# Performance work log

Hardware: AMD Instinct MI355X
Metric: run time of the kernel (lower is better)

## Reference

```python
import jax, jax.numpy as jnp
import numpy as np


def setup_inputs() -> dict:
    key = jax.random.key(0)
    ks = jax.random.split(key, 7)
    B, T, N, D, K = 64, 1024, 512, 64, 80
    return {
        "review_seq": jax.random.normal(ks[0], (B, T, D), dtype=jnp.float32),
        "post_seq": jax.random.normal(ks[1], (B, N, D), dtype=jnp.float32),
        "Wl": jax.random.normal(ks[2], (D, D), dtype=jnp.float32) * 0.05,
        "Wr": jax.random.normal(ks[3], (K, D), dtype=jnp.float32) * 0.05,
        "Wp": jax.random.normal(ks[4], (K, D), dtype=jnp.float32) * 0.05,
        "whr": jax.random.normal(ks[5], (1, K), dtype=jnp.float32) * 0.05,
        "whp": jax.random.normal(ks[6], (1, K), dtype=jnp.float32) * 0.05,
    }


def reference(review_seq, post_seq, Wl, Wr, Wp, whr, whp):
    # Affinity matrix: L[b,t,n] = tanh(review[b,t,:] @ Wl @ post[b,n,:])
    L = jnp.tanh(jnp.einsum('btd,dD,bnD->btn', review_seq, Wl, post_seq))
    # Co-attention hidden maps (k x seq)
    Hp = jnp.tanh(jnp.einsum('kd,bnd->bkn', Wp, post_seq)
                  + jnp.einsum('kd,btd,btn->bkn', Wr, review_seq, L))
    Hr = jnp.tanh(jnp.einsum('kd,btd->bkt', Wr, review_seq)
                  + jnp.einsum('kd,bnd,btn->bkt', Wp, post_seq, L))
    # Attention weights over post (n) and review (t) positions
    Ap = jax.nn.softmax(jnp.einsum('k,bkn->bn', whp[0], Hp), axis=-1)
    Ar = jax.nn.softmax(jnp.einsum('k,bkt->bt', whr[0], Hr), axis=-1)
    # Attention-weighted pooling
    co_p = jnp.einsum('bnd,bn->bd', post_seq, Ap)
    co_r = jnp.einsum('btd,bt->bd', review_seq, Ar)
    return jnp.concatenate([co_p, co_r], axis=1)  # [B, 2*D]
```

## Files before the change

kernel.cpp:

```cpp
#include <hip/hip_runtime.h>
#include <hip/hip_bf16.h>
#include <cstdint>

#define DEV __device__ __forceinline__

constexpr int B = 64, T = 1024, N = 512, D = 64, K = 80;

typedef __attribute__((ext_vector_type(8))) short bf16x8;
typedef __attribute__((ext_vector_type(4))) float f32x4;

DEV float fast_tanh(float x) {
    x = fminf(fmaxf(x, -15.f), 15.f);
    float e = __expf(2.f * x);
    return 1.f - 2.f * __builtin_amdgcn_rcpf(e + 1.f);
}

DEV unsigned short f2bf(float f) {
    unsigned int u = __float_as_uint(f);
    unsigned int r = (u + 0x7fffu + ((u >> 16) & 1u)) >> 16;
    return (unsigned short)r;
}
DEV float bf2f(unsigned short s) {
    return __uint_as_float(((unsigned int)s) << 16);
}

DEV unsigned short cvt_bf16(float v) {
    __hip_bfloat16 h = __float2bfloat16(v);
    return *reinterpret_cast<unsigned short*>(&h);
}

DEV void gload16(const unsigned short* src, unsigned short* dst) {
    __builtin_amdgcn_global_load_lds(
        (const __attribute__((address_space(1))) void*)src,
        (__attribute__((address_space(3))) void*)dst,
        16, 0, 0);
}

DEV size_t tix(size_t row, int col, int S8) {
    return (((row >> 4) * S8 + (size_t)(col >> 3)) << 7) + ((row & 15) << 3) + (col & 7);
}

#define MFMA(a, b, c) __builtin_amdgcn_mfma_f32_16x16x32_bf16((a), (b), (c), 0, 0, 0)


DEV void matWl_body(int bid, char* lds, const float* __restrict__ review,
                    const float* __restrict__ Wl,
                    unsigned short* __restrict__ Mhi, unsigned short* __restrict__ Mlo) {
    float (*Wls)[64] = reinterpret_cast<float(*)[64]>(lds);
    float (*Rs)[64]  = reinterpret_cast<float(*)[64]>(lds + 16384);
    int tid = threadIdx.x;
    size_t base = (size_t)bid * 4096;
#pragma unroll
    for (int i = 0; i < 16; i++) {
        int e = tid + i * 256;
        Wls[e >> 6][e & 63] = Wl[e];
        Rs[e >> 6][e & 63] = review[base + e];
    }
    __syncthreads();
    int c = tid & 63, r0 = tid >> 6;
    float acc[16];
#pragma unroll
    for (int i = 0; i < 16; i++) acc[i] = 0.f;
    for (int d = 0; d < 64; d += 2) {
        float w0 = Wls[d][c], w1 = Wls[d + 1][c];
#pragma unroll
        for (int i = 0; i < 16; i++)
            acc[i] += Rs[r0 * 16 + i][d] * w0 + Rs[r0 * 16 + i][d + 1] * w1;
    }
#pragma unroll
    for (int i = 0; i < 16; i++) {
        size_t row = (size_t)bid * 64 + r0 * 16 + i;
        size_t o = tix(row, c, 8);
        unsigned short h = f2bf(acc[i]);
        Mhi[o] = h;
        Mlo[o] = f2bf(acc[i] - bf2f(h));
    }
}

DEV void split_body(int bid, const float* __restrict__ X,
                    unsigned short* __restrict__ Xhi, unsigned short* __restrict__ Xlo) {
    int i = bid * 256 + threadIdx.x;
    float4 v = *reinterpret_cast<const float4*>(X + (size_t)i * 4);
    ushort4 h, lo;
    h.x = f2bf(v.x); lo.x = f2bf(v.x - bf2f(h.x));
    h.y = f2bf(v.y); lo.y = f2bf(v.y - bf2f(h.y));
    h.z = f2bf(v.z); lo.z = f2bf(v.z - bf2f(h.z));
    h.w = f2bf(v.w); lo.w = f2bf(v.w - bf2f(h.w));
    size_t o = tix((size_t)(i >> 4), (i & 15) * 4, 8);
    *reinterpret_cast<ushort4*>(Xhi + o) = h;
    *reinterpret_cast<ushort4*>(Xlo + o) = lo;
}

DEV void proj_body(int sx, int b, char* lds, const float* __restrict__ W,
                   const float* __restrict__ X,
                   unsigned short* __restrict__ Phi, unsigned short* __restrict__ Plo, int S) {
    float (*Ws)[64] = reinterpret_cast<float(*)[64]>(lds);
    float (*Xs)[65] = reinterpret_cast<float(*)[65]>(lds + 20480);
    int tid = threadIdx.x, tx = tid & 63, ty = tid >> 6;
    int s0 = sx * 64;
#pragma unroll
    for (int i = 0; i < 20; i++) { int e = tid + i * 256; Ws[e >> 6][e & 63] = W[e]; }
    const float* Xp = X + ((size_t)b * S + s0) * 64;
#pragma unroll
    for (int i = 0; i < 16; i++) { int e = tid + i * 256; Xs[e >> 6][e & 63] = Xp[e]; }
    __syncthreads();
    float acc[20];
#pragma unroll
    for (int kk = 0; kk < 20; kk++) acc[kk] = 0.f;
    for (int d = 0; d < 64; d += 4) {
        float x0 = Xs[tx][d], x1 = Xs[tx][d + 1], x2 = Xs[tx][d + 2], x3 = Xs[tx][d + 3];
#pragma unroll
        for (int kk = 0; kk < 20; kk++) {
            const float4 w = *reinterpret_cast<const float4*>(&Ws[ty * 20 + kk][d]);
            acc[kk] += w.x * x0 + w.y * x1 + w.z * x2 + w.w * x3;
        }
    }
    int S8 = S >> 3;
#pragma unroll
    for (int kk = 0; kk < 20; kk++) {
        size_t idx = tix((size_t)b * K + ty * 20 + kk, s0 + tx, S8);
        float v = acc[kk];
        unsigned short h = f2bf(v);
        Phi[idx] = h;
        Plo[idx] = f2bf(v - bf2f(h));
    }
}

__global__ __launch_bounds__(256) void k_prelude(
    const float* __restrict__ review, const float* __restrict__ post,
    const float* __restrict__ Wl, const float* __restrict__ Wr,
    const float* __restrict__ Wp,
    unsigned short* __restrict__ Mhi, unsigned short* __restrict__ Mlo,
    unsigned short* __restrict__ PsH, unsigned short* __restrict__ PsL,
    unsigned short* __restrict__ Rhi, unsigned short* __restrict__ Rlo,
    unsigned short* __restrict__ Phi, unsigned short* __restrict__ Plo,
    float* __restrict__ out) {
    __shared__ __align__(16) char lds[37120];
    int bid = blockIdx.x;
    if (bid < 1024) {
        matWl_body(bid, lds, review, Wl, Mhi, Mlo);
    } else if (bid < 3072) {
        split_body(bid - 1024, post, PsH, PsL);
    } else if (bid < 4096) {
        int i = bid - 3072;
        proj_body(i & 15, i >> 4, lds, Wr, review, Rhi, Rlo, T);
    } else if (bid < 4608) {
        int i = bid - 4096;
        proj_body(i & 7, i >> 3, lds, Wp, post, Phi, Plo, N);
    } else {
        int i = bid - 4608;
        out[(size_t)i * 256 + threadIdx.x] = 0.f;
    }
}


DEV void hp_body(int b, int nc0, unsigned short* smem,
                 const unsigned short* __restrict__ Mhi, const unsigned short* __restrict__ Mlo,
                 const unsigned short* __restrict__ PsH, const unsigned short* __restrict__ PsL,
                 const unsigned short* __restrict__ Rhi, const unsigned short* __restrict__ Rlo,
                 const unsigned short* __restrict__ Phi, const unsigned short* __restrict__ Plo,
                 const float* __restrict__ whp, float* __restrict__ logits_p) {
    unsigned short* MH_l = smem;
    unsigned short* ML_l = smem + 4096;
    unsigned short* RH_l = smem + 8192;
    unsigned short* RL_l = smem + 13312;
    typedef unsigned short LtRow[72];
    LtRow* Lt = reinterpret_cast<LtRow*>(smem + 18432);
    int tid = threadIdx.x, l = tid & 63, wv = tid >> 6;
    int lr = l & 15, lg = l >> 4;

    size_t prow = (size_t)b * N + nc0 + wv * 16 + lr;
    size_t p0 = tix(prow, lg * 8, 8), p1 = tix(prow, 32 + lg * 8, 8);
    bf16x8 pah0 = *reinterpret_cast<const bf16x8*>(PsH + p0);
    bf16x8 pah1 = *reinterpret_cast<const bf16x8*>(PsH + p1);
    bf16x8 pal0 = *reinterpret_cast<const bf16x8*>(PsL + p0);
    bf16x8 pal1 = *reinterpret_cast<const bf16x8*>(PsL + p1);

    const unsigned short* srcp[9];
    unsigned short* dstp[9];
    int strd[9];
#pragma unroll
    for (int i = 0; i < 9; i++) {
        int c = wv + i * 4;
        if (c < 8) {
            srcp[i] = Mhi + (size_t)b * T * 64 + c * 512;
            dstp[i] = MH_l + c * 512;
            strd[i] = 4096;
        } else if (c < 16) {
            srcp[i] = Mlo + (size_t)b * T * 64 + (c - 8) * 512;
            dstp[i] = ML_l + (c - 8) * 512;
            strd[i] = 4096;
        } else {
            int j = c - 16, jj = (j < 10) ? j : j - 10;
            int rg = jj >> 1, half = jj & 1;
            srcp[i] = ((j < 10) ? Rhi : Rlo) + (size_t)(b * 5 + rg) * 16384 + half * 512;
            dstp[i] = ((j < 10) ? RH_l : RL_l) + rg * 1024 + half * 512;
            strd[i] = 1024;
        }
        srcp[i] += l * 8;
    }

    f32x4 hp[5];
#pragma unroll
    for (int f = 0; f < 5; f++) hp[f] = (f32x4){0.f, 0.f, 0.f, 0.f};

#pragma unroll
    for (int i = 0; i < 4; i++) { gload16(srcp[i], dstp[i]); srcp[i] += strd[i]; }
    __syncthreads();
#pragma unroll
    for (int i = 4; i < 9; i++) { gload16(srcp[i], dstp[i]); srcp[i] += strd[i]; }

    for (int tt = 0; tt < 16; tt++) {
#pragma unroll
        for (int tf = 0; tf < 4; tf++) {
            int o0 = tf * 1024 + lg * 128 + lr * 8;
            int o1 = tf * 1024 + (4 + lg) * 128 + lr * 8;
            bf16x8 mh0 = *reinterpret_cast<const bf16x8*>(MH_l + o0);
            bf16x8 mh1 = *reinterpret_cast<const bf16x8*>(MH_l + o1);
            bf16x8 ml0 = *reinterpret_cast<const bf16x8*>(ML_l + o0);
            bf16x8 ml1 = *reinterpret_cast<const bf16x8*>(ML_l + o1);
            f32x4 a = (f32x4){0.f, 0.f, 0.f, 0.f};
            a = MFMA(pah0, mh0, a);
            a = MFMA(pah0, ml0, a);
            a = MFMA(pal0, mh0, a);
            a = MFMA(pah1, mh1, a);
            a = MFMA(pah1, ml1, a);
            a = MFMA(pal1, mh1, a);
#pragma unroll
            for (int r = 0; r < 4; r++)
                Lt[wv * 16 + lg * 4 + r][tf * 16 + lr] = cvt_bf16(fast_tanh(a[r]));
        }
        __syncthreads();
        if (tt < 15) {
#pragma unroll
            for (int i = 0; i < 4; i++) { gload16(srcp[i], dstp[i]); srcp[i] += strd[i]; }
        }
        bf16x8 bt0 = *reinterpret_cast<const bf16x8*>(&Lt[wv * 16 + lr][lg * 8]);
        bf16x8 bt1 = *reinterpret_cast<const bf16x8*>(&Lt[wv * 16 + lr][32 + lg * 8]);
#pragma unroll
        for (int kf = 0; kf < 5; kf++) {
            int o0 = kf * 1024 + lg * 128 + lr * 8;
            int o1 = kf * 1024 + (4 + lg) * 128 + lr * 8;
            bf16x8 rh0 = *reinterpret_cast<const bf16x8*>(RH_l + o0);
            bf16x8 rh1 = *reinterpret_cast<const bf16x8*>(RH_l + o1);
            bf16x8 rl0 = *reinterpret_cast<const bf16x8*>(RL_l + o0);
            bf16x8 rl1 = *reinterpret_cast<const bf16x8*>(RL_l + o1);
            hp[kf] = MFMA(rh0, bt0, hp[kf]);
            hp[kf] = MFMA(rl0, bt0, hp[kf]);
            hp[kf] = MFMA(rh1, bt1, hp[kf]);
            hp[kf] = MFMA(rl1, bt1, hp[kf]);
        }
        __syncthreads();
        if (tt < 15) {
#pragma unroll
            for (int i = 4; i < 9; i++) { gload16(srcp[i], dstp[i]); srcp[i] += strd[i]; }
        }
    }

    int n = nc0 + wv * 16 + lr;
    float partial = 0.f;
#pragma unroll
    for (int kf = 0; kf < 5; kf++)
#pragma unroll
        for (int r = 0; r < 4; r++) {
            int k = kf * 16 + lg * 4 + r;
            size_t idx = tix((size_t)b * K + k, n, 64);
            float pp = bf2f(Phi[idx]) + bf2f(Plo[idx]);
            partial += whp[k] * fast_tanh(pp + hp[kf][r]);
        }
    partial += __shfl_xor(partial, 16);
    partial += __shfl_xor(partial, 32);
    if (lg == 0) logits_p[(size_t)b * N + n] = partial;
}

DEV void hr_body(int b, int tc0, unsigned short* smem,
                 const unsigned short* __restrict__ Mhi, const unsigned short* __restrict__ Mlo,
                 const unsigned short* __restrict__ PsH, const unsigned short* __restrict__ PsL,
                 const unsigned short* __restrict__ Phi, const unsigned short* __restrict__ Plo,
                 const unsigned short* __restrict__ Rhi, const unsigned short* __restrict__ Rlo,
                 const float* __restrict__ whr, float* __restrict__ logits_r) {
    unsigned short* PsH_l = smem;
    unsigned short* PsL_l = smem + 4096;
    unsigned short* PpH_l = smem + 8192;
    unsigned short* PpL_l = smem + 13312;
    typedef unsigned short LtRow[72];
    LtRow* Lt = reinterpret_cast<LtRow*>(smem + 18432);
    int tid = threadIdx.x, l = tid & 63, wv = tid >> 6;
    int lr = l & 15, lg = l >> 4;

    size_t mrow = (size_t)b * T + tc0 + wv * 16 + lr;
    size_t m0 = tix(mrow, lg * 8, 8), m1 = tix(mrow, 32 + lg * 8, 8);
    bf16x8 mh0 = *reinterpret_cast<const bf16x8*>(Mhi + m0);
    bf16x8 mh1 = *reinterpret_cast<const bf16x8*>(Mhi + m1);
    bf16x8 ml0 = *reinterpret_cast<const bf16x8*>(Mlo + m0);
    bf16x8 ml1 = *reinterpret_cast<const bf16x8*>(Mlo + m1);

    const unsigned short* srcp[9];
    unsigned short* dstp[9];
    int strd[9];
#pragma unroll
    for (int i = 0; i < 9; i++) {
        int c = wv + i * 4;
        if (c < 8) {
            srcp[i] = PsH + (size_t)b * N * 64 + c * 512;
            dstp[i] = PsH_l + c * 512;
            strd[i] = 4096;
        } else if (c < 16) {
            srcp[i] = PsL + (size_t)b * N * 64 + (c - 8) * 512;
            dstp[i] = PsL_l + (c - 8) * 512;
            strd[i] = 4096;
        } else {
            int j = c - 16, jj = (j < 10) ? j : j - 10;
            int rg = jj >> 1, half = jj & 1;
            srcp[i] = ((j < 10) ? Phi : Plo) + (size_t)(b * 5 + rg) * 8192 + half * 512;
            dstp[i] = ((j < 10) ? PpH_l : PpL_l) + rg * 1024 + half * 512;
            strd[i] = 1024;
        }
        srcp[i] += l * 8;
    }

    f32x4 hr[5];
#pragma unroll
    for (int f = 0; f < 5; f++) hr[f] = (f32x4){0.f, 0.f, 0.f, 0.f};

#pragma unroll
    for (int i = 0; i < 4; i++) { gload16(srcp[i], dstp[i]); srcp[i] += strd[i]; }
    __syncthreads();
#pragma unroll
    for (int i = 4; i < 9; i++) { gload16(srcp[i], dstp[i]); srcp[i] += strd[i]; }

    for (int nt = 0; nt < 8; nt++) {
#pragma unroll
        for (int nf = 0; nf < 4; nf++) {
            int o0 = nf * 1024 + lg * 128 + lr * 8;
            int o1 = nf * 1024 + (4 + lg) * 128 + lr * 8;
            bf16x8 ph0 = *reinterpret_cast<const bf16x8*>(PsH_l + o0);
            bf16x8 ph1 = *reinterpret_cast<const bf16x8*>(PsH_l + o1);
            bf16x8 pl0 = *reinterpret_cast<const bf16x8*>(PsL_l + o0);
            bf16x8 pl1 = *reinterpret_cast<const bf16x8*>(PsL_l + o1);
            f32x4 a = (f32x4){0.f, 0.f, 0.f, 0.f};
            a = MFMA(mh0, ph0, a);
            a = MFMA(mh0, pl0, a);
            a = MFMA(ml0, ph0, a);
            a = MFMA(mh1, ph1, a);
            a = MFMA(mh1, pl1, a);
            a = MFMA(ml1, ph1, a);
#pragma unroll
            for (int r = 0; r < 4; r++)
                Lt[wv * 16 + lg * 4 + r][nf * 16 + lr] = cvt_bf16(fast_tanh(a[r]));
        }
        __syncthreads();
        if (nt < 7) {
#pragma unroll
            for (int i = 0; i < 4; i++) { gload16(srcp[i], dstp[i]); srcp[i] += strd[i]; }
        }
        bf16x8 bt0 = *reinterpret_cast<const bf16x8*>(&Lt[wv * 16 + lr][lg * 8]);
        bf16x8 bt1 = *reinterpret_cast<const bf16x8*>(&Lt[wv * 16 + lr][32 + lg * 8]);
#pragma unroll
        for (int kf = 0; kf < 5; kf++) {
            int o0 = kf * 1024 + lg * 128 + lr * 8;
            int o1 = kf * 1024 + (4 + lg) * 128 + lr * 8;
            bf16x8 qh0 = *reinterpret_cast<const bf16x8*>(PpH_l + o0);
            bf16x8 qh1 = *reinterpret_cast<const bf16x8*>(PpH_l + o1);
            bf16x8 ql0 = *reinterpret_cast<const bf16x8*>(PpL_l + o0);
            bf16x8 ql1 = *reinterpret_cast<const bf16x8*>(PpL_l + o1);
            hr[kf] = MFMA(qh0, bt0, hr[kf]);
            hr[kf] = MFMA(ql0, bt0, hr[kf]);
            hr[kf] = MFMA(qh1, bt1, hr[kf]);
            hr[kf] = MFMA(ql1, bt1, hr[kf]);
        }
        __syncthreads();
        if (nt < 7) {
#pragma unroll
            for (int i = 4; i < 9; i++) { gload16(srcp[i], dstp[i]); srcp[i] += strd[i]; }
        }
    }

    int t = tc0 + wv * 16 + lr;
    float partial = 0.f;
#pragma unroll
    for (int kf = 0; kf < 5; kf++)
#pragma unroll
        for (int r = 0; r < 4; r++) {
            int k = kf * 16 + lg * 4 + r;
            size_t idx = tix((size_t)b * K + k, t, 128);
            float rr = bf2f(Rhi[idx]) + bf2f(Rlo[idx]);
            partial += whr[k] * fast_tanh(rr + hr[kf][r]);
        }
    partial += __shfl_xor(partial, 16);
    partial += __shfl_xor(partial, 32);
    if (lg == 0) logits_r[(size_t)b * T + t] = partial;
}

__global__ __launch_bounds__(256) void k_fused(
    const unsigned short* __restrict__ Mhi, const unsigned short* __restrict__ Mlo,
    const unsigned short* __restrict__ PsH, const unsigned short* __restrict__ PsL,
    const unsigned short* __restrict__ Rhi, const unsigned short* __restrict__ Rlo,
    const unsigned short* __restrict__ Phi, const unsigned short* __restrict__ Plo,
    const float* __restrict__ whp, const float* __restrict__ whr,
    float* __restrict__ logits_p, float* __restrict__ logits_r) {
    __shared__ __align__(16) unsigned short smem[23040];
    int lin = blockIdx.x;
    int x = lin & 7, j = lin >> 3;
    int bg = j / 24, role = j - bg * 24;
    int b = bg * 8 + x;
    if (role < 8) {
        hp_body(b, role * 64, smem, Mhi, Mlo, PsH, PsL, Rhi, Rlo, Phi, Plo, whp, logits_p);
    } else {
        hr_body(b, (role - 8) * 64, smem, Mhi, Mlo, PsH, PsL, Phi, Plo, Rhi, Rlo, whr, logits_r);
    }
}

DEV void softpool_body(const float* __restrict__ logits, const float* __restrict__ X,
                       float* __restrict__ out, int S, int off, int cy,
                       float* sm, float* red) {
    int b = blockIdx.x, tid = threadIdx.x;
    int c0 = cy * 128;
    for (int i = tid; i < S; i += 256) sm[i] = logits[(size_t)b * S + i];
    __syncthreads();
    float m = -1e30f;
    for (int i = tid; i < S; i += 256) m = fmaxf(m, sm[i]);
    red[tid] = m;
    __syncthreads();
    for (int s = 128; s > 0; s >>= 1) {
        if (tid < s) red[tid] = fmaxf(red[tid], red[tid + s]);
        __syncthreads();
    }
    float mx = red[0];
    __syncthreads();
    float psum = 0.f;
    for (int i = tid; i < S; i += 256) {
        float e = __expf(sm[i] - mx);
        sm[i] = e;
        psum += e;
    }
    red[tid] = psum;
    __syncthreads();
    for (int s = 128; s > 0; s >>= 1) {
        if (tid < s) red[tid] += red[tid + s];
        __syncthreads();
    }
    float inv = 1.f / red[0];
    __syncthreads();
    int d = tid & 63, g = tid >> 6;
    float acc = 0.f;
    for (int n = c0 + g; n < c0 + 128; n += 4) acc += sm[n] * X[((size_t)b * S + n) * 64 + d];
    red[tid] = acc * inv;
    __syncthreads();
    if (g == 0)
        atomicAdd(&out[(size_t)b * 128 + off + d],
                  red[d] + red[64 + d] + red[128 + d] + red[192 + d]);
}

__global__ __launch_bounds__(256) void k_softpool2(
    const float* __restrict__ logits_p, const float* __restrict__ logits_r,
    const float* __restrict__ post, const float* __restrict__ review,
    float* __restrict__ out) {
    __shared__ float sm[1024];
    __shared__ float red[256];
    int y = blockIdx.y;
    if (y < N / 128) softpool_body(logits_p, post, out, N, 0, y, sm, red);
    else             softpool_body(logits_r, review, out, T, 64, y - N / 128, sm, red);
}

extern "C" void kernel_launch(void* const* d_in, const int* in_sizes, int n_in,
                              void* d_out, int out_size, void* d_ws, size_t ws_size,
                              hipStream_t stream) {
    const float* review = (const float*)d_in[0];
    const float* post   = (const float*)d_in[1];
    const float* Wl     = (const float*)d_in[2];
    const float* Wr     = (const float*)d_in[3];
    const float* Wp     = (const float*)d_in[4];
    const float* whr    = (const float*)d_in[5];
    const float* whp    = (const float*)d_in[6];
    float* out = (float*)d_out;

    char* p = (char*)d_ws;
    unsigned short* Mhi = (unsigned short*)p;  p += (size_t)B * T * D * 2;
    unsigned short* Mlo = (unsigned short*)p;  p += (size_t)B * T * D * 2;
    unsigned short* PsH = (unsigned short*)p;  p += (size_t)B * N * D * 2;
    unsigned short* PsL = (unsigned short*)p;  p += (size_t)B * N * D * 2;
    unsigned short* Rhi = (unsigned short*)p;  p += (size_t)B * K * T * 2;
    unsigned short* Rlo = (unsigned short*)p;  p += (size_t)B * K * T * 2;
    unsigned short* Phi = (unsigned short*)p;  p += (size_t)B * K * N * 2;
    unsigned short* Plo = (unsigned short*)p;  p += (size_t)B * K * N * 2;
    float* logits_p = (float*)p;        p += (size_t)B * N * 4;
    float* logits_r = (float*)p;        p += (size_t)B * T * 4;

    k_prelude<<<dim3(4640), dim3(256), 0, stream>>>(review, post, Wl, Wr, Wp,
                                                    Mhi, Mlo, PsH, PsL, Rhi, Rlo,
                                                    Phi, Plo, out);
    k_fused<<<dim3(1536), dim3(256), 0, stream>>>(Mhi, Mlo, PsH, PsL, Rhi, Rlo,
                                                  Phi, Plo, whp, whr, logits_p, logits_r);
    k_softpool2<<<dim3(B, 12), dim3(256), 0, stream>>>(logits_p, logits_r, post, review, out);
}
```

Baseline: 139.3 us.

## Fuse softmax pooling into main kernel via last-block counter; add MFMA priority hints

Removes the separate softmax-pool launch. Each batch's 24 blocks in the fused kernel increment a per-batch counter, and the last block to finish computes both softmax poolings for that batch and writes the output directly, with no atomics on the output. The prelude now zeroes the counters instead of the output. s_setprio hints are also placed around the MFMA sections to raise wave priority during compute. The cost is that the pooling work is serialized in a single block per batch, which may create a tail at the end of the kernel.

Result: slower. 353.1 us (+153.5%).

```diff
diff --git a/kernel.cpp b/kernel.cpp
--- a/kernel.cpp
+++ b/kernel.cpp
@@ -134,7 +134,7 @@
     unsigned short* __restrict__ PsH, unsigned short* __restrict__ PsL,
     unsigned short* __restrict__ Rhi, unsigned short* __restrict__ Rlo,
     unsigned short* __restrict__ Phi, unsigned short* __restrict__ Plo,
-    float* __restrict__ out) {
+    int* __restrict__ cnt) {
     __shared__ __align__(16) char lds[37120];
     int bid = blockIdx.x;
     if (bid < 1024) {
@@ -148,8 +148,7 @@
         int i = bid - 4096;
         proj_body(i & 7, i >> 3, lds, Wp, post, Phi, Plo, N);
     } else {
-        int i = bid - 4608;
-        out[(size_t)i * 256 + threadIdx.x] = 0.f;
+        if (threadIdx.x < 64) cnt[threadIdx.x] = 0;
     }
 }
 
@@ -211,6 +210,7 @@
     for (int i = 4; i < 9; i++) { gload16(srcp[i], dstp[i]); srcp[i] += strd[i]; }
 
     for (int tt = 0; tt < 16; tt++) {
+        __builtin_amdgcn_s_setprio(1);
 #pragma unroll
         for (int tf = 0; tf < 4; tf++) {
             int o0 = tf * 1024 + lg * 128 + lr * 8;
@@ -230,6 +230,7 @@
             for (int r = 0; r < 4; r++)
                 Lt[wv * 16 + lg * 4 + r][tf * 16 + lr] = cvt_bf16(fast_tanh(a[r]));
         }
+        __builtin_amdgcn_s_setprio(0);
         __syncthreads();
         if (tt < 15) {
 #pragma unroll
@@ -237,6 +238,7 @@
         }
         bf16x8 bt0 = *reinterpret_cast<const bf16x8*>(&Lt[wv * 16 + lr][lg * 8]);
         bf16x8 bt1 = *reinterpret_cast<const bf16x8*>(&Lt[wv * 16 + lr][32 + lg * 8]);
+        __builtin_amdgcn_s_setprio(1);
 #pragma unroll
         for (int kf = 0; kf < 5; kf++) {
             int o0 = kf * 1024 + lg * 128 + lr * 8;
@@ -250,6 +252,7 @@
             hp[kf] = MFMA(rh1, bt1, hp[kf]);
             hp[kf] = MFMA(rl1, bt1, hp[kf]);
         }
+        __builtin_amdgcn_s_setprio(0);
         __syncthreads();
         if (tt < 15) {
 #pragma unroll
@@ -330,6 +333,7 @@
     for (int i = 4; i < 9; i++) { gload16(srcp[i], dstp[i]); srcp[i] += strd[i]; }
 
     for (int nt = 0; nt < 8; nt++) {
+        __builtin_amdgcn_s_setprio(1);
 #pragma unroll
         for (int nf = 0; nf < 4; nf++) {
             int o0 = nf * 1024 + lg * 128 + lr * 8;
@@ -349,6 +353,7 @@
             for (int r = 0; r < 4; r++)
                 Lt[wv * 16 + lg * 4 + r][nf * 16 + lr] = cvt_bf16(fast_tanh(a[r]));
         }
+        __builtin_amdgcn_s_setprio(0);
         __syncthreads();
         if (nt < 7) {
 #pragma unroll
@@ -356,6 +361,7 @@
         }
         bf16x8 bt0 = *reinterpret_cast<const bf16x8*>(&Lt[wv * 16 + lr][lg * 8]);
         bf16x8 bt1 = *reinterpret_cast<const bf16x8*>(&Lt[wv * 16 + lr][32 + lg * 8]);
+        __builtin_amdgcn_s_setprio(1);
 #pragma unroll
         for (int kf = 0; kf < 5; kf++) {
             int o0 = kf * 1024 + lg * 128 + lr * 8;
@@ -369,6 +375,7 @@
             hr[kf] = MFMA(qh1, bt1, hr[kf]);
             hr[kf] = MFMA(ql1, bt1, hr[kf]);
         }
+        __builtin_amdgcn_s_setprio(0);
         __syncthreads();
         if (nt < 7) {
 #pragma unroll
@@ -390,6 +397,45 @@
     partial += __shfl_xor(partial, 16);
     partial += __shfl_xor(partial, 32);
     if (lg == 0) logits_r[(size_t)b * T + t] = partial;
+}
+
+DEV void pool_one(int b, const float* __restrict__ logits, const float* __restrict__ X,
+                  float* __restrict__ out, int S, int off, float* sm, float* red) {
+    int tid = threadIdx.x;
+    for (int i = tid; i < S; i += 256) sm[i] = logits[(size_t)b * S + i];
+    __syncthreads();
+    float m = -1e30f;
+    for (int i = tid; i < S; i += 256) m = fmaxf(m, sm[i]);
+    red[tid] = m;
+    __syncthreads();
+    for (int s = 128; s > 0; s >>= 1) {
+        if (tid < s) red[tid] = fmaxf(red[tid], red[tid + s]);
+        __syncthreads();
+    }
+    float mx = red[0];
+    __syncthreads();
+    float psum = 0.f;
+    for (int i = tid; i < S; i += 256) {
+        float e = __expf(sm[i] - mx);
+        sm[i] = e;
+        psum += e;
+    }
+    red[tid] = psum;
+    __syncthreads();
+    for (int s = 128; s > 0; s >>= 1) {
+        if (tid < s) red[tid] += red[tid + s];
+        __syncthreads();
+    }
+    float inv = 1.f / red[0];
+    __syncthreads();
+    int d = tid & 63, g = tid >> 6;
+    float acc = 0.f;
+    for (int n = g; n < S; n += 4) acc += sm[n] * X[((size_t)b * S + n) * 64 + d];
+    red[tid] = acc * inv;
+    __syncthreads();
+    if (g == 0)
+        out[(size_t)b * 128 + off + d] = red[d] + red[64 + d] + red[128 + d] + red[192 + d];
+    __syncthreads();
 }
 
 __global__ __launch_bounds__(256) void k_fused(
@@ -398,8 +444,11 @@
     const unsigned short* __restrict__ Rhi, const unsigned short* __restrict__ Rlo,
     const unsigned short* __restrict__ Phi, const unsigned short* __restrict__ Plo,
     const float* __restrict__ whp, const float* __restrict__ whr,
-    float* __restrict__ logits_p, float* __restrict__ logits_r) {
+    float* __restrict__ logits_p, float* __restrict__ logits_r,
+    const float* __restrict__ post, const float* __restrict__ review,
+    int* __restrict__ cnt, float* __restrict__ out) {
     __shared__ __align__(16) unsigned short smem[23040];
+    __shared__ int lastFlag;
     int lin = blockIdx.x;
     int x = lin & 7, j = lin >> 3;
     int bg = j / 24, role = j - bg * 24;
@@ -409,58 +458,20 @@
     } else {
         hr_body(b, (role - 8) * 64, smem, Mhi, Mlo, PsH, PsL, Phi, Plo, Rhi, Rlo, whr, logits_r);
     }
-}
-
-DEV void softpool_body(const float* __restrict__ logits, const float* __restrict__ X,
-                       float* __restrict__ out, int S, int off, int cy,
-                       float* sm, float* red) {
-    int b = blockIdx.x, tid = threadIdx.x;
-    int c0 = cy * 128;
-    for (int i = tid; i < S; i += 256) sm[i] = logits[(size_t)b * S + i];
-    __syncthreads();
-    float m = -1e30f;
-    for (int i = tid; i < S; i += 256) m = fmaxf(m, sm[i]);
-    red[tid] = m;
-    __syncthreads();
-    for (int s = 128; s > 0; s >>= 1) {
-        if (tid < s) red[tid] = fmaxf(red[tid], red[tid + s]);
-        __syncthreads();
-    }
-    float mx = red[0];
-    __syncthreads();
-    float psum = 0.f;
-    for (int i = tid; i < S; i += 256) {
-        float e = __expf(sm[i] - mx);
-        sm[i] = e;
-        psum += e;
-    }
-    red[tid] = psum;
-    __syncthreads();
-    for (int s = 128; s > 0; s >>= 1) {
-        if (tid < s) red[tid] += red[tid + s];
-        __syncthreads();
-    }
-    float inv = 1.f / red[0];
-    __syncthreads();
-    int d = tid & 63, g = tid >> 6;
-    float acc = 0.f;
-    for (int n = c0 + g; n < c0 + 128; n += 4) acc += sm[n] * X[((size_t)b * S + n) * 64 + d];
-    red[tid] = acc * inv;
-    __syncthreads();
-    if (g == 0)
-        atomicAdd(&out[(size_t)b * 128 + off + d],
-                  red[d] + red[64 + d] + red[128 + d] + red[192 + d]);
-}
-
-__global__ __launch_bounds__(256) void k_softpool2(
-    const float* __restrict__ logits_p, const float* __restrict__ logits_r,
-    const float* __restrict__ post, const float* __restrict__ review,
-    float* __restrict__ out) {
-    __shared__ float sm[1024];
-    __shared__ float red[256];
-    int y = blockIdx.y;
-    if (y < N / 128) softpool_body(logits_p, post, out, N, 0, y, sm, red);
-    else             softpool_body(logits_r, review, out, T, 64, y - N / 128, sm, red);
+
+    __threadfence();
+    if (threadIdx.x == 0) {
+        int old = atomicAdd(&cnt[b], 1);
+        lastFlag = (old == 23);
+    }
+    __syncthreads();
+    if (lastFlag) {
+        __threadfence();
+        float* sm = reinterpret_cast<float*>(smem);
+        float* red = sm + 1024;
+        pool_one(b, logits_p, post, out, N, 0, sm, red);
+        pool_one(b, logits_r, review, out, T, 64, sm, red);
+    }
 }
 
 extern "C" void kernel_launch(void* const* d_in, const int* in_sizes, int n_in,
@@ -486,11 +497,12 @@
     unsigned short* Plo = (unsigned short*)p;  p += (size_t)B * K * N * 2;
     float* logits_p = (float*)p;        p += (size_t)B * N * 4;
     float* logits_r = (float*)p;        p += (size_t)B * T * 4;
-
-    k_prelude<<<dim3(4640), dim3(256), 0, stream>>>(review, post, Wl, Wr, Wp,
+    int* cnt = (int*)p;                 p += 256;
+
+    k_prelude<<<dim3(4609), dim3(256), 0, stream>>>(review, post, Wl, Wr, Wp,
                                                     Mhi, Mlo, PsH, PsL, Rhi, Rlo,
-                                                    Phi, Plo, out);
+                                                    Phi, Plo, cnt);
     k_fused<<<dim3(1536), dim3(256), 0, stream>>>(Mhi, Mlo, PsH, PsL, Rhi, Rlo,
-                                                  Phi, Plo, whp, whr, logits_p, logits_r);
-    k_softpool2<<<dim3(B, 12), dim3(256), 0, stream>>>(logits_p, logits_r, post, review, out);
-}
+                                                  Phi, Plo, whp, whr, logits_p, logits_r,
+                                                  post, review, cnt, out);
+}
```
